# Optimization experiments

Measured on AMD Instinct MI355X. Metric: run time of the kernel, lower is better.

## Reference

```python
import jax, jax.numpy as jnp
import numpy as np

NEG_INF = -1e30

def masked_softmax(logits, mask, axis):
    # mask broadcastable to logits; 1 = keep, 0 = mask out
    masked = jnp.where(mask > 0, logits, NEG_INF)
    return jax.nn.softmax(masked, axis=axis)

def setup_inputs() -> dict:
    key = jax.random.key(0)
    ks = jax.random.split(key, 6)
    B, H, C, Q = 64, 128, 1024, 128
    c = jax.random.normal(ks[0], (B, H, C), dtype=jnp.float32)
    q = jax.random.normal(ks[1], (B, H, Q), dtype=jnp.float32)
    c_mask = jnp.ones((B, C), dtype=jnp.float32)
    q_mask = jnp.ones((B, Q), dtype=jnp.float32)
    # xavier_uniform for (H,1): bound = sqrt(6/(H+1))
    bnd_v = float(np.sqrt(6.0 / (H + 1)))
    context_weights = jax.random.uniform(ks[2], (H, 1), minval=-bnd_v, maxval=bnd_v, dtype=jnp.float32)
    query_weights = jax.random.uniform(ks[3], (H, 1), minval=-bnd_v, maxval=bnd_v, dtype=jnp.float32)
    # xavier_uniform for (1,1,H): fan_in=1, fan_out=H -> bound = sqrt(6/(1+H))
    cq_weights = jax.random.uniform(ks[4], (1, 1, H), minval=-bnd_v, maxval=bnd_v, dtype=jnp.float32)
    bias = jnp.zeros((1,), dtype=jnp.float32)
    return {"c": c, "q": q, "c_mask": c_mask, "q_mask": q_mask,
            "context_weights": context_weights, "query_weights": query_weights,
            "cq_weights": cq_weights, "bias": bias}

def reference(c, q, c_mask, q_mask, context_weights, query_weights, cq_weights, bias):
    # to (B, len, H)
    c = jnp.swapaxes(c, 1, 2)  # (B, c_len, H)
    q = jnp.swapaxes(q, 1, 2)  # (B, q_len, H)
    B, c_len, H = c.shape
    q_len = q.shape[1]
    # trilinear similarity: (B, c_len, q_len)
    s0 = c @ context_weights                         # (B, c_len, 1)
    s1 = jnp.swapaxes(q @ query_weights, 1, 2)       # (B, 1, q_len)
    s2 = jnp.einsum('bch,bqh->bcq', c * cq_weights, q)
    S = s0 + s1 + s2 + bias
    a_att = masked_softmax(S, q_mask[:, None, :], axis=2)  # softmax over q_len
    b_att = masked_softmax(S, c_mask[:, :, None], axis=1)  # softmax over c_len
    a = jnp.einsum('bcq,bqh->bch', a_att, q)
    b = jnp.einsum('bcq,bkq,bkh->bch', a_att, b_att, c)
    x = jnp.concatenate([c, a, c * a, c * b], axis=2)  # (B, c_len, 4H)
    return jnp.swapaxes(x, 1, 2)  # (B, 4H, c_len)
```

## Files before the change

### kernel.cpp

```cpp
#include <hip/hip_runtime.h>
#include <math.h>

#define NEG_HUGE -1e30f
constexpr int B_ = 64, H_ = 128, C_ = 1024, Q_ = 128;

typedef __bf16 bf16x8 __attribute__((ext_vector_type(8)));
typedef float f32x4 __attribute__((ext_vector_type(4)));
typedef short short8 __attribute__((ext_vector_type(8)));
typedef short short4s __attribute__((ext_vector_type(4)));

__device__ __forceinline__ float bs2f(short s) {
  unsigned u = ((unsigned)(unsigned short)s) << 16;
  float f; __builtin_memcpy(&f, &u, 4); return f;
}
__device__ __forceinline__ short f2bs(float f) {
  unsigned u; __builtin_memcpy(&u, &f, 4);
  u = (u + 0x7fffu + ((u >> 16) & 1u)) >> 16;
  return (short)u;
}
__device__ __forceinline__ void nts4(float* p, float4 v) {
  f32x4 x; x[0] = v.x; x[1] = v.y; x[2] = v.z; x[3] = v.w;
  __builtin_nontemporal_store(x, (f32x4*)p);
}

__global__ __launch_bounds__(256) void kq(const float* __restrict__ qin,
                                          const float* __restrict__ qw,
                                          const float* __restrict__ cqw,
                                          const float* __restrict__ qmask,
                                          short* __restrict__ qTw,
                                          short* __restrict__ qbf,
                                          float* __restrict__ s1m) {
  __shared__ float T[64 * 130];
  const int t = threadIdx.x;
  const int q0 = blockIdx.x * 64, b = blockIdx.y;
#pragma unroll
  for (int p = 0; p < 8; ++p) {
    int fidx = t + 256 * p;
    int h = fidx >> 4, seg = fidx & 15;
    float4 v = *(const float4*)&qin[(b * H_ + h) * Q_ + q0 + seg * 4];
    T[(seg * 4 + 0) * 130 + h] = v.x;
    T[(seg * 4 + 1) * 130 + h] = v.y;
    T[(seg * 4 + 2) * 130 + h] = v.z;
    T[(seg * 4 + 3) * 130 + h] = v.w;
    short4s o; o[0] = f2bs(v.x); o[1] = f2bs(v.y); o[2] = f2bs(v.z); o[3] = f2bs(v.w);
    *(short4s*)&qbf[(b * H_ + h) * Q_ + q0 + seg * 4] = o;
  }
  __syncthreads();
  if (t < 64) {
    float acc = 0.f;
#pragma unroll 8
    for (int h = 0; h < 128; ++h) acc += T[t * 130 + h] * qw[h];
    float qm = (qmask[b * Q_ + q0 + t] > 0.f) ? 0.f : NEG_HUGE;
    s1m[b * Q_ + q0 + t] = acc + qm;
  }
  {
    const int q = t >> 2, off = t & 3;
    short* dst = qTw + (b * Q_ + q0 + q) * H_;
#pragma unroll
    for (int j = 0; j < 4; ++j) {
      int hbv = off * 32 + j * 8;
      short8 v;
#pragma unroll
      for (int i = 0; i < 8; ++i) v[i] = f2bs(T[q * 130 + hbv + i] * cqw[hbv + i]);
      *(short8*)&dst[hbv] = v;
    }
  }
}

__global__ __launch_bounds__(256) void k1_mfma(
    const float* __restrict__ cin, const short* __restrict__ qTw,
    const float* __restrict__ s1m, const float* __restrict__ cmask,
    const float* __restrict__ ctxw,
    short* __restrict__ a_att, short* __restrict__ ePT,
    short* __restrict__ cbf,
    float* __restrict__ pcm, float* __restrict__ pcs) {
  __shared__ __align__(16) char uni[65536];
  short* AL = (short*)uni;
  short* BL = (short*)(uni + 32768);
  short* RP = (short*)uni;
  __shared__ float s1mL[128], scolL[128], pw[512], mpL[128], s0part[2][128];

  const int t = threadIdx.x;
  const int w = t >> 6, l = t & 63, quad = l >> 4, lcol = l & 15;
  const int b = blockIdx.x, bx = blockIdx.y, c0 = bx * 128;

  if (t < 128) s1mL[t] = s1m[b * Q_ + t];

  {
    const int cl = t & 127, hw = t >> 7;
    float s0c = 0.f;
#pragma unroll
    for (int it = 0; it < 8; ++it) {
      const int hb = hw + it * 2;
      const float* sp = cin + ((size_t)(b * H_ + hb * 8)) * C_ + c0 + cl;
      short* cb = cbf + ((size_t)(b * H_ + hb * 8)) * C_ + c0 + cl;
      short8 o;
#pragma unroll
      for (int i = 0; i < 8; ++i) {
        float f = sp[(size_t)i * C_];
        o[i] = f2bs(f);
        s0c += f * ctxw[hb * 8 + i];
        cb[(size_t)i * C_] = o[i];
      }
      *(short8*)&AL[cl * 128 + 8 * (hb ^ (cl & 7))] = o;
    }
    s0part[hw][cl] = s0c;
  }
  {
    const int q = t >> 1, hb0 = (t & 1) * 8;
#pragma unroll
    for (int i = 0; i < 8; ++i) {
      const int hb = hb0 + i;
      *(short8*)&BL[q * 128 + 8 * (hb ^ (q & 7))] =
          *(const short8*)&qTw[(b * Q_ + q) * H_ + hb * 8];
    }
  }
  __syncthreads();
  if (t < 128) {
    float cm = (cmask[b * C_ + c0 + t] > 0.f) ? 0.f : NEG_HUGE;
    scolL[t] = cm + s0part[0][t] + s0part[1][t];
  }

  f32x4 acc[2][8];
#pragma unroll
  for (int mt = 0; mt < 2; ++mt)
#pragma unroll
    for (int nt = 0; nt < 8; ++nt) acc[mt][nt] = (f32x4){0.f, 0.f, 0.f, 0.f};

#pragma unroll
  for (int kc = 0; kc < 4; ++kc) {
    const int kb = kc * 4 + quad;
    const int sw = 8 * (kb ^ (lcol & 7));
    bf16x8 af0 = *(bf16x8*)&AL[(w * 32 + lcol) * 128 + sw];
    bf16x8 af1 = *(bf16x8*)&AL[(w * 32 + 16 + lcol) * 128 + sw];
#pragma unroll
    for (int nt = 0; nt < 8; ++nt) {
      bf16x8 bfrag = *(bf16x8*)&BL[(nt * 16 + lcol) * 128 + sw];
      acc[0][nt] = __builtin_amdgcn_mfma_f32_16x16x32_bf16(af0, bfrag, acc[0][nt], 0, 0, 0);
      acc[1][nt] = __builtin_amdgcn_mfma_f32_16x16x32_bf16(af1, bfrag, acc[1][nt], 0, 0, 0);
    }
  }
  __syncthreads();

  float s1v[8];
#pragma unroll
  for (int nt = 0; nt < 8; ++nt) s1v[nt] = s1mL[nt * 16 + lcol];
  float cs0[2][4];
#pragma unroll
  for (int mt = 0; mt < 2; ++mt)
#pragma unroll
    for (int r = 0; r < 4; ++r)
      cs0[mt][r] = scolL[w * 32 + mt * 16 + quad * 4 + r];

  float rm[2][4];
#pragma unroll
  for (int mt = 0; mt < 2; ++mt)
#pragma unroll
    for (int r = 0; r < 4; ++r) {
      float m = -INFINITY;
#pragma unroll
      for (int nt = 0; nt < 8; ++nt) m = fmaxf(m, acc[mt][nt][r] + s1v[nt]);
      rm[mt][r] = m;
    }
#pragma unroll
  for (int d = 1; d <= 8; d <<= 1)
#pragma unroll
    for (int mt = 0; mt < 2; ++mt)
#pragma unroll
      for (int r = 0; r < 4; ++r)
        rm[mt][r] = fmaxf(rm[mt][r], __shfl_xor(rm[mt][r], d));

  float pmv[8];
#pragma unroll
  for (int nt = 0; nt < 8; ++nt) {
    float m = -INFINITY;
#pragma unroll
    for (int mt = 0; mt < 2; ++mt)
#pragma unroll
      for (int r = 0; r < 4; ++r) m = fmaxf(m, acc[mt][nt][r] + cs0[mt][r]);
    pmv[nt] = m;
  }
#pragma unroll
  for (int nt = 0; nt < 8; ++nt) {
    pmv[nt] = fmaxf(pmv[nt], __shfl_xor(pmv[nt], 16));
    pmv[nt] = fmaxf(pmv[nt], __shfl_xor(pmv[nt], 32));
  }
  if (l < 16) {
#pragma unroll
    for (int nt = 0; nt < 8; ++nt) pw[w * 128 + nt * 16 + lcol] = pmv[nt];
  }

#pragma unroll
  for (int mt = 0; mt < 2; ++mt)
#pragma unroll
    for (int nt = 0; nt < 8; ++nt)
#pragma unroll
      for (int r = 0; r < 4; ++r)
        acc[mt][nt][r] = __expf(acc[mt][nt][r] + s1v[nt] - rm[mt][r]);

  float inv[2][4];
#pragma unroll
  for (int mt = 0; mt < 2; ++mt)
#pragma unroll
    for (int r = 0; r < 4; ++r) {
      float s = 0.f;
#pragma unroll
      for (int nt = 0; nt < 8; ++nt) s += acc[mt][nt][r];
      inv[mt][r] = s;
    }
#pragma unroll
  for (int d = 1; d <= 8; d <<= 1)
#pragma unroll
    for (int mt = 0; mt < 2; ++mt)
#pragma unroll
      for (int r = 0; r < 4; ++r)
        inv[mt][r] += __shfl_xor(inv[mt][r], d);
#pragma unroll
  for (int mt = 0; mt < 2; ++mt)
#pragma unroll
    for (int r = 0; r < 4; ++r) inv[mt][r] = 1.f / inv[mt][r];

#pragma unroll
  for (int mt = 0; mt < 2; ++mt)
#pragma unroll
    for (int nt = 0; nt < 8; ++nt)
#pragma unroll
      for (int r = 0; r < 4; ++r) {
        int row = w * 32 + mt * 16 + quad * 4 + r;
        int col = nt * 16 + lcol;
        RP[row * 136 + col] = f2bs(acc[mt][nt][r] * inv[mt][r]);
      }
  __syncthreads();
  {
    const int row = t >> 1, half = t & 1;
    short* dst = a_att + (b * C_ + c0 + row) * Q_ + half * 64;
    const short* srcp = RP + row * 136 + half * 64;
#pragma unroll
    for (int j = 0; j < 8; ++j) *(short8*)&dst[j * 8] = *(const short8*)&srcp[j * 8];
  }
  __syncthreads();
  if (t < 128) {
    float m = fmaxf(fmaxf(pw[t], pw[128 + t]), fmaxf(pw[256 + t], pw[384 + t]));
    mpL[t] = m;
    pcm[(b * 8 + bx) * Q_ + t] = m;
  }
  __syncthreads();
  float mpv[8];
#pragma unroll
  for (int nt = 0; nt < 8; ++nt) mpv[nt] = mpL[nt * 16 + lcol];

  float crm[2][4];
#pragma unroll
  for (int mt = 0; mt < 2; ++mt)
#pragma unroll
    for (int r = 0; r < 4; ++r) crm[mt][r] = cs0[mt][r] + rm[mt][r];
  float psv[8];
#pragma unroll
  for (int nt = 0; nt < 8; ++nt) {
    const float sm = s1v[nt] + mpv[nt];
    const int qq = nt * 16 + lcol;
    float s = 0.f;
#pragma unroll
    for (int mt = 0; mt < 2; ++mt)
#pragma unroll
      for (int r = 0; r < 4; ++r) {
        float v = acc[mt][nt][r] * __expf(crm[mt][r] - sm);
        s += v;
        RP[qq * 136 + (w * 32 + mt * 16 + quad * 4 + r)] = f2bs(v);
      }
    psv[nt] = s;
  }
#pragma unroll
  for (int nt = 0; nt < 8; ++nt) {
    psv[nt] += __shfl_xor(psv[nt], 16);
    psv[nt] += __shfl_xor(psv[nt], 32);
  }
  if (l < 16) {
#pragma unroll
    for (int nt = 0; nt < 8; ++nt) pw[w * 128 + nt * 16 + lcol] = psv[nt];
  }
  __syncthreads();
  if (t < 128) pcs[(b * 8 + bx) * Q_ + t] = pw[t] + pw[128 + t] + pw[256 + t] + pw[384 + t];
  {
    const int qq = t >> 1, half = t & 1;
    short* dst = ePT + (b * Q_ + qq) * C_ + c0 + half * 64;
    const short* srcp = RP + qq * 136 + half * 64;
#pragma unroll
    for (int j = 0; j < 8; ++j) *(short8*)&dst[j * 8] = *(const short8*)&srcp[j * 8];
  }
}

__global__ __launch_bounds__(256) void k3_T(
    const short* __restrict__ ePT, const short* __restrict__ cbf,
    const float* __restrict__ pcm, const float* __restrict__ pcs,
    short* __restrict__ TmT) {
  __shared__ __align__(16) char uni[36864];
  short* AL = (short*)uni;
  short* BL = (short*)(uni + 4096);
  short* RP = (short*)uni;
  __shared__ float scT[8][128];
  __shared__ float icL[128];
  const int t = threadIdx.x;
  const int w = t >> 6, l = t & 63, quad = l >> 4, lcol = l & 15;
  const int b = blockIdx.x, qg = blockIdx.y * 16;

  if (t < 128) {
    float m[8]; float M = -INFINITY;
#pragma unroll
    for (int k = 0; k < 8; ++k) { m[k] = pcm[(b * 8 + k) * Q_ + t]; M = fmaxf(M, m[k]); }
    float s = 0.f;
#pragma unroll
    for (int k = 0; k < 8; ++k) {
      float e = __expf(m[k] - M);
      scT[k][t] = e;
      s += pcs[(b * 8 + k) * Q_ + t] * e;
    }
    icL[t] = 1.f / s;
  }

  f32x4 acc[2];
  acc[0] = (f32x4){0.f, 0.f, 0.f, 0.f};
  acc[1] = (f32x4){0.f, 0.f, 0.f, 0.f};

  const int qa = t >> 4, cs = t & 15;
  const int hh = t >> 4;
  __syncthreads();

  for (int ck = 0; ck < 8; ++ck) {
    {
      const float sA = scT[ck][qg + qa];
      short8 v = *(const short8*)&ePT[(b * Q_ + qg + qa) * C_ + ck * 128 + cs * 8];
      short8 o;
#pragma unroll
      for (int j = 0; j < 8; ++j) o[j] = f2bs(bs2f(v[j]) * sA);
      *(short8*)&AL[qa * 128 + 8 * (cs ^ (qa & 7))] = o;
    }
#pragma unroll
    for (int p = 0; p < 8; ++p) {
      const int h = p * 16 + hh;
      *(short8*)&BL[h * 128 + 8 * (cs ^ (h & 7))] =
          *(const short8*)&cbf[(b * H_ + h) * C_ + ck * 128 + cs * 8];
    }
    __syncthreads();
#pragma unroll
    for (int ks = 0; ks < 4; ++ks) {
      const int kb = ks * 4 + quad;
      bf16x8 af = *(bf16x8*)&AL[lcol * 128 + 8 * (kb ^ (lcol & 7))];
#pragma unroll
      for (int nt = 0; nt < 2; ++nt) {
        const int hr = w * 32 + nt * 16 + lcol;
        bf16x8 bfrag = *(bf16x8*)&BL[hr * 128 + 8 * (kb ^ (hr & 7))];
        acc[nt] = __builtin_amdgcn_mfma_f32_16x16x32_bf16(af, bfrag, acc[nt], 0, 0, 0);
      }
    }
    __syncthreads();
  }
#pragma unroll
  for (int nt = 0; nt < 2; ++nt)
#pragma unroll
    for (int r = 0; r < 4; ++r) {
      const int qi = quad * 4 + r;
      RP[(w * 32 + nt * 16 + lcol) * 16 + qi] = f2bs(acc[nt][r] * icL[qg + qi]);
    }
  __syncthreads();
  {
    const int h = t >> 1, half = t & 1;
    *(short8*)&TmT[(b * H_ + h) * Q_ + qg + half * 8] =
        *(const short8*)&RP[h * 16 + half * 8];
  }
}

__global__ __launch_bounds__(256) void k4_out(
    const short* __restrict__ a_att, const short* __restrict__ qbf,
    const short* __restrict__ TmT, const float* __restrict__ cin,
    float* __restrict__ out) {
  __shared__ __align__(16) char uni[34816];
  short* AL = (short*)uni;
  short* B1 = (short*)(uni + 10240);
  short* B2 = (short*)(uni + 15360);
  float* RPF = (float*)uni;
  const int t = threadIdx.x;
  const int w = t >> 6, l = t & 63, quad = l >> 4, lcol = l & 15;
  const int b = blockIdx.x, hb = blockIdx.y * 64, c0 = blockIdx.z * 128;

  f32x4 accA[2][4], accB[2][4];
#pragma unroll
  for (int mt = 0; mt < 2; ++mt)
#pragma unroll
    for (int nt = 0; nt < 4; ++nt) {
      accA[mt][nt] = (f32x4){0.f, 0.f, 0.f, 0.f};
      accB[mt][nt] = (f32x4){0.f, 0.f, 0.f, 0.f};
    }

  const int ar = t >> 2, aoff = t & 3;
  for (int kc = 0; kc < 4; ++kc) {
    const int q0 = kc * 32;
    *(short8*)&AL[ar * 40 + aoff * 8] =
        *(const short8*)&a_att[(b * C_ + c0 + ar) * Q_ + q0 + aoff * 8];
    *(short8*)&AL[(64 + ar) * 40 + aoff * 8] =
        *(const short8*)&a_att[(b * C_ + c0 + 64 + ar) * Q_ + q0 + aoff * 8];
    *(short8*)&B1[ar * 40 + aoff * 8] =
        *(const short8*)&qbf[(b * H_ + hb + ar) * Q_ + q0 + aoff * 8];
    *(short8*)&B2[ar * 40 + aoff * 8] =
        *(const short8*)&TmT[(b * H_ + hb + ar) * Q_ + q0 + aoff * 8];
    __syncthreads();
    bf16x8 af0 = *(bf16x8*)&AL[(w * 32 + lcol) * 40 + quad * 8];
    bf16x8 af1 = *(bf16x8*)&AL[(w * 32 + 16 + lcol) * 40 + quad * 8];
#pragma unroll
    for (int nt = 0; nt < 4; ++nt) {
      bf16x8 bq = *(bf16x8*)&B1[(nt * 16 + lcol) * 40 + quad * 8];
      bf16x8 bt = *(bf16x8*)&B2[(nt * 16 + lcol) * 40 + quad * 8];
      accA[0][nt] = __builtin_amdgcn_mfma_f32_16x16x32_bf16(af0, bq, accA[0][nt], 0, 0, 0);
      accA[1][nt] = __builtin_amdgcn_mfma_f32_16x16x32_bf16(af1, bq, accA[1][nt], 0, 0, 0);
      accB[0][nt] = __builtin_amdgcn_mfma_f32_16x16x32_bf16(af0, bt, accB[0][nt], 0, 0, 0);
      accB[1][nt] = __builtin_amdgcn_mfma_f32_16x16x32_bf16(af1, bt, accB[1][nt], 0, 0, 0);
    }
    __syncthreads();
  }

  const int lr = t >> 5, coln = (t & 31) * 4;
  float* ob = out + (size_t)b * 512 * 1024;
  float4 cvv[8];

#pragma unroll
  for (int mt = 0; mt < 2; ++mt)
#pragma unroll
    for (int nt = 0; nt < 4; ++nt)
#pragma unroll
      for (int r = 0; r < 4; ++r)
        RPF[(nt * 16 + lcol) * 136 + (w * 32 + mt * 16 + quad * 4 + r)] = accA[mt][nt][r];
  __syncthreads();
#pragma unroll
  for (int iter = 0; iter < 8; ++iter) {
    int hl = iter * 8 + lr;
    int hrow = hb + hl;
    float4 la = *(float4*)&RPF[hl * 136 + coln];
    float4 cv = *(const float4*)&cin[(b * H_ + hrow) * C_ + c0 + coln];
    cvv[iter] = cv;
    nts4(&ob[(size_t)hrow * 1024 + c0 + coln], cv);
    nts4(&ob[(size_t)(128 + hrow) * 1024 + c0 + coln], la);
    float4 p = make_float4(cv.x * la.x, cv.y * la.y, cv.z * la.z, cv.w * la.w);
    nts4(&ob[(size_t)(256 + hrow) * 1024 + c0 + coln], p);
  }
  __syncthreads();
#pragma unroll
  for (int mt = 0; mt < 2; ++mt)
#pragma unroll
    for (int nt = 0; nt < 4; ++nt)
#pragma unroll
      for (int r = 0; r < 4; ++r)
        RPF[(nt * 16 + lcol) * 136 + (w * 32 + mt * 16 + quad * 4 + r)] = accB[mt][nt][r];
  __syncthreads();
#pragma unroll
  for (int iter = 0; iter < 8; ++iter) {
    int hl = iter * 8 + lr;
    int hrow = hb + hl;
    float4 lb = *(float4*)&RPF[hl * 136 + coln];
    float4 cv = cvv[iter];
    float4 p = make_float4(cv.x * lb.x, cv.y * lb.y, cv.z * lb.z, cv.w * lb.w);
    nts4(&ob[(size_t)(384 + hrow) * 1024 + c0 + coln], p);
  }
}

extern "C" void kernel_launch(void* const* d_in, const int* in_sizes, int n_in,
                              void* d_out, int out_size, void* d_ws, size_t ws_size,
                              hipStream_t stream) {
  const float* c     = (const float*)d_in[0];
  const float* q     = (const float*)d_in[1];
  const float* cmask = (const float*)d_in[2];
  const float* qmask = (const float*)d_in[3];
  const float* ctxw  = (const float*)d_in[4];
  const float* qw    = (const float*)d_in[5];
  const float* cqw   = (const float*)d_in[6];
  float* out = (float*)d_out;

  char* ws = (char*)d_ws;
  short* qTw    = (short*)(ws);
  short* qbf    = (short*)(ws + 2097152);
  short* a_att  = (short*)(ws + 4194304);
  short* ePT    = (short*)(ws + 20971520);
  short* cbf    = (short*)(ws + 37748736);
  short* TmT    = (short*)(ws + 54525952);
  float* s1m    = (float*)(ws + 56623104);
  float* pcm    = (float*)(ws + 56655872);
  float* pcs    = (float*)(ws + 56918016);

  kq<<<dim3(2, B_), dim3(256), 0, stream>>>(q, qw, cqw, qmask, qTw, qbf, s1m);
  k1_mfma<<<dim3(B_, 8), dim3(256), 0, stream>>>(c, qTw, s1m, cmask, ctxw,
                                                 a_att, ePT, cbf, pcm, pcs);
  k3_T<<<dim3(B_, 8), dim3(256), 0, stream>>>(ePT, cbf, pcm, pcs, TmT);
  k4_out<<<dim3(B_, 2, 8), dim3(256), 0, stream>>>(a_att, qbf, TmT, c, out);
}
```

Baseline: 226.4 us.

## Enlarge k3 and k4 tiles to cut redundant operand reloads

k3_T now uses 512-thread blocks that each cover 32 query columns instead of 16, so every cbf tile loaded into shared memory feeds twice as many MFMAs and the number of blocks halves. k4_out now covers all 128 hidden rows per block instead of 64, so each a_att tile is loaded once per c-chunk rather than twice. In exchange there are fewer blocks (256 for k3, 512 for k4), which can hurt occupancy and latency hiding. k4 also carries twice as many accumulator registers and reads the input c a second time for the c*b output instead of caching it in registers.

Measured after the change: 238.0 us. 5.1% more time.

```diff
diff --git a/kernel.cpp b/kernel.cpp
--- a/kernel.cpp
+++ b/kernel.cpp
@@ -290,19 +290,20 @@
   }
 }
 
-__global__ __launch_bounds__(256) void k3_T(
+__global__ __launch_bounds__(512) void k3_T(
     const short* __restrict__ ePT, const short* __restrict__ cbf,
     const float* __restrict__ pcm, const float* __restrict__ pcs,
     short* __restrict__ TmT) {
-  __shared__ __align__(16) char uni[36864];
+  __shared__ __align__(16) char uni[40960];
   short* AL = (short*)uni;
-  short* BL = (short*)(uni + 4096);
+  short* BL = (short*)(uni + 8192);
   short* RP = (short*)uni;
   __shared__ float scT[8][128];
   __shared__ float icL[128];
   const int t = threadIdx.x;
   const int w = t >> 6, l = t & 63, quad = l >> 4, lcol = l & 15;
-  const int b = blockIdx.x, qg = blockIdx.y * 16;
+  const int b = blockIdx.x, qg = blockIdx.y * 32;
+  const int qgw = (w >> 2) * 16, hg = (w & 3) * 32;
 
   if (t < 128) {
     float m[8]; float M = -INFINITY;
@@ -323,7 +324,7 @@
   acc[1] = (f32x4){0.f, 0.f, 0.f, 0.f};
 
   const int qa = t >> 4, cs = t & 15;
-  const int hh = t >> 4;
+  const int hb0 = t >> 4, sb = t & 15;
   __syncthreads();
 
   for (int ck = 0; ck < 8; ++ck) {
@@ -336,19 +337,20 @@
       *(short8*)&AL[qa * 128 + 8 * (cs ^ (qa & 7))] = o;
     }
 #pragma unroll
-    for (int p = 0; p < 8; ++p) {
-      const int h = p * 16 + hh;
-      *(short8*)&BL[h * 128 + 8 * (cs ^ (h & 7))] =
-          *(const short8*)&cbf[(b * H_ + h) * C_ + ck * 128 + cs * 8];
+    for (int p = 0; p < 4; ++p) {
+      const int h = p * 32 + hb0;
+      *(short8*)&BL[h * 128 + 8 * (sb ^ (h & 7))] =
+          *(const short8*)&cbf[(b * H_ + h) * C_ + ck * 128 + sb * 8];
     }
     __syncthreads();
 #pragma unroll
     for (int ks = 0; ks < 4; ++ks) {
       const int kb = ks * 4 + quad;
-      bf16x8 af = *(bf16x8*)&AL[lcol * 128 + 8 * (kb ^ (lcol & 7))];
+      const int ar = qgw + lcol;
+      bf16x8 af = *(bf16x8*)&AL[ar * 128 + 8 * (kb ^ (ar & 7))];
 #pragma unroll
       for (int nt = 0; nt < 2; ++nt) {
-        const int hr = w * 32 + nt * 16 + lcol;
+        const int hr = hg + nt * 16 + lcol;
         bf16x8 bfrag = *(bf16x8*)&BL[hr * 128 + 8 * (kb ^ (hr & 7))];
         acc[nt] = __builtin_amdgcn_mfma_f32_16x16x32_bf16(af, bfrag, acc[nt], 0, 0, 0);
       }
@@ -359,14 +361,13 @@
   for (int nt = 0; nt < 2; ++nt)
 #pragma unroll
     for (int r = 0; r < 4; ++r) {
-      const int qi = quad * 4 + r;
-      RP[(w * 32 + nt * 16 + lcol) * 16 + qi] = f2bs(acc[nt][r] * icL[qg + qi]);
+      const int qi = qgw + quad * 4 + r;
+      RP[(hg + nt * 16 + lcol) * 32 + qi] = f2bs(acc[nt][r] * icL[qg + qi]);
     }
   __syncthreads();
   {
-    const int h = t >> 1, half = t & 1;
-    *(short8*)&TmT[(b * H_ + h) * Q_ + qg + half * 8] =
-        *(const short8*)&RP[h * 16 + half * 8];
+    const int h = t >> 2, qo = (t & 3) * 8;
+    *(short8*)&TmT[(b * H_ + h) * Q_ + qg + qo] = *(const short8*)&RP[h * 32 + qo];
   }
 }
 
@@ -377,17 +378,17 @@
   __shared__ __align__(16) char uni[34816];
   short* AL = (short*)uni;
   short* B1 = (short*)(uni + 10240);
-  short* B2 = (short*)(uni + 15360);
+  short* B2 = (short*)(uni + 20480);
   float* RPF = (float*)uni;
   const int t = threadIdx.x;
   const int w = t >> 6, l = t & 63, quad = l >> 4, lcol = l & 15;
-  const int b = blockIdx.x, hb = blockIdx.y * 64, c0 = blockIdx.z * 128;
-
-  f32x4 accA[2][4], accB[2][4];
-#pragma unroll
-  for (int mt = 0; mt < 2; ++mt)
-#pragma unroll
-    for (int nt = 0; nt < 4; ++nt) {
+  const int b = blockIdx.x, c0 = blockIdx.y * 128;
+
+  f32x4 accA[2][8], accB[2][8];
+#pragma unroll
+  for (int mt = 0; mt < 2; ++mt)
+#pragma unroll
+    for (int nt = 0; nt < 8; ++nt) {
       accA[mt][nt] = (f32x4){0.f, 0.f, 0.f, 0.f};
       accB[mt][nt] = (f32x4){0.f, 0.f, 0.f, 0.f};
     }
@@ -400,14 +401,18 @@
     *(short8*)&AL[(64 + ar) * 40 + aoff * 8] =
         *(const short8*)&a_att[(b * C_ + c0 + 64 + ar) * Q_ + q0 + aoff * 8];
     *(short8*)&B1[ar * 40 + aoff * 8] =
-        *(const short8*)&qbf[(b * H_ + hb + ar) * Q_ + q0 + aoff * 8];
+        *(const short8*)&qbf[(b * H_ + ar) * Q_ + q0 + aoff * 8];
+    *(short8*)&B1[(64 + ar) * 40 + aoff * 8] =
+        *(const short8*)&qbf[(b * H_ + 64 + ar) * Q_ + q0 + aoff * 8];
     *(short8*)&B2[ar * 40 + aoff * 8] =
-        *(const short8*)&TmT[(b * H_ + hb + ar) * Q_ + q0 + aoff * 8];
+        *(const short8*)&TmT[(b * H_ + ar) * Q_ + q0 + aoff * 8];
+    *(short8*)&B2[(64 + ar) * 40 + aoff * 8] =
+        *(const short8*)&TmT[(b * H_ + 64 + ar) * Q_ + q0 + aoff * 8];
     __syncthreads();
     bf16x8 af0 = *(bf16x8*)&AL[(w * 32 + lcol) * 40 + quad * 8];
     bf16x8 af1 = *(bf16x8*)&AL[(w * 32 + 16 + lcol) * 40 + quad * 8];
 #pragma unroll
-    for (int nt = 0; nt < 4; ++nt) {
+    for (int nt = 0; nt < 8; ++nt) {
       bf16x8 bq = *(bf16x8*)&B1[(nt * 16 + lcol) * 40 + quad * 8];
       bf16x8 bt = *(bf16x8*)&B2[(nt * 16 + lcol) * 40 + quad * 8];
       accA[0][nt] = __builtin_amdgcn_mfma_f32_16x16x32_bf16(af0, bq, accA[0][nt], 0, 0, 0);
@@ -420,45 +425,52 @@
 
   const int lr = t >> 5, coln = (t & 31) * 4;
   float* ob = out + (size_t)b * 512 * 1024;
-  float4 cvv[8];
-
-#pragma unroll
-  for (int mt = 0; mt < 2; ++mt)
-#pragma unroll
-    for (int nt = 0; nt < 4; ++nt)
-#pragma unroll
-      for (int r = 0; r < 4; ++r)
-        RPF[(nt * 16 + lcol) * 136 + (w * 32 + mt * 16 + quad * 4 + r)] = accA[mt][nt][r];
-  __syncthreads();
-#pragma unroll
-  for (int iter = 0; iter < 8; ++iter) {
-    int hl = iter * 8 + lr;
-    int hrow = hb + hl;
-    float4 la = *(float4*)&RPF[hl * 136 + coln];
-    float4 cv = *(const float4*)&cin[(b * H_ + hrow) * C_ + c0 + coln];
-    cvv[iter] = cv;
-    nts4(&ob[(size_t)hrow * 1024 + c0 + coln], cv);
-    nts4(&ob[(size_t)(128 + hrow) * 1024 + c0 + coln], la);
-    float4 p = make_float4(cv.x * la.x, cv.y * la.y, cv.z * la.z, cv.w * la.w);
-    nts4(&ob[(size_t)(256 + hrow) * 1024 + c0 + coln], p);
-  }
-  __syncthreads();
-#pragma unroll
-  for (int mt = 0; mt < 2; ++mt)
-#pragma unroll
-    for (int nt = 0; nt < 4; ++nt)
-#pragma unroll
-      for (int r = 0; r < 4; ++r)
-        RPF[(nt * 16 + lcol) * 136 + (w * 32 + mt * 16 + quad * 4 + r)] = accB[mt][nt][r];
-  __syncthreads();
-#pragma unroll
-  for (int iter = 0; iter < 8; ++iter) {
-    int hl = iter * 8 + lr;
-    int hrow = hb + hl;
-    float4 lb = *(float4*)&RPF[hl * 136 + coln];
-    float4 cv = cvv[iter];
-    float4 p = make_float4(cv.x * lb.x, cv.y * lb.y, cv.z * lb.z, cv.w * lb.w);
-    nts4(&ob[(size_t)(384 + hrow) * 1024 + c0 + coln], p);
+
+#pragma unroll
+  for (int hh = 0; hh < 2; ++hh) {
+#pragma unroll
+    for (int mt = 0; mt < 2; ++mt)
+#pragma unroll
+      for (int n4 = 0; n4 < 4; ++n4)
+#pragma unroll
+        for (int r = 0; r < 4; ++r)
+          RPF[(n4 * 16 + lcol) * 136 + (w * 32 + mt * 16 + quad * 4 + r)] =
+              accA[mt][hh * 4 + n4][r];
+    __syncthreads();
+#pragma unroll
+    for (int iter = 0; iter < 8; ++iter) {
+      int hl = iter * 8 + lr;
+      int hrow = hh * 64 + hl;
+      float4 la = *(float4*)&RPF[hl * 136 + coln];
+      float4 cv = *(const float4*)&cin[(b * H_ + hrow) * C_ + c0 + coln];
+      nts4(&ob[(size_t)hrow * 1024 + c0 + coln], cv);
+      nts4(&ob[(size_t)(128 + hrow) * 1024 + c0 + coln], la);
+      float4 p = make_float4(cv.x * la.x, cv.y * la.y, cv.z * la.z, cv.w * la.w);
+      nts4(&ob[(size_t)(256 + hrow) * 1024 + c0 + coln], p);
+    }
+    __syncthreads();
+  }
+#pragma unroll
+  for (int hh = 0; hh < 2; ++hh) {
+#pragma unroll
+    for (int mt = 0; mt < 2; ++mt)
+#pragma unroll
+      for (int n4 = 0; n4 < 4; ++n4)
+#pragma unroll
+        for (int r = 0; r < 4; ++r)
+          RPF[(n4 * 16 + lcol) * 136 + (w * 32 + mt * 16 + quad * 4 + r)] =
+              accB[mt][hh * 4 + n4][r];
+    __syncthreads();
+#pragma unroll
+    for (int iter = 0; iter < 8; ++iter) {
+      int hl = iter * 8 + lr;
+      int hrow = hh * 64 + hl;
+      float4 lb = *(float4*)&RPF[hl * 136 + coln];
+      float4 cv = *(const float4*)&cin[(b * H_ + hrow) * C_ + c0 + coln];
+      float4 p = make_float4(cv.x * lb.x, cv.y * lb.y, cv.z * lb.z, cv.w * lb.w);
+      nts4(&ob[(size_t)(384 + hrow) * 1024 + c0 + coln], p);
+    }
+    __syncthreads();
   }
 }
 
@@ -488,6 +500,6 @@
   kq<<<dim3(2, B_), dim3(256), 0, stream>>>(q, qw, cqw, qmask, qTw, qbf, s1m);
   k1_mfma<<<dim3(B_, 8), dim3(256), 0, stream>>>(c, qTw, s1m, cmask, ctxw,
                                                  a_att, ePT, cbf, pcm, pcs);
-  k3_T<<<dim3(B_, 8), dim3(256), 0, stream>>>(ePT, cbf, pcm, pcs, TmT);
-  k4_out<<<dim3(B_, 2, 8), dim3(256), 0, stream>>>(a_att, qbf, TmT, c, out);
-}
+  k3_T<<<dim3(B_, 4), dim3(512), 0, stream>>>(ePT, cbf, pcm, pcs, TmT);
+  k4_out<<<dim3(B_, 8), dim3(256), 0, stream>>>(a_att, qbf, TmT, c, out);
+}
```
